# Performance work log

Measured on AMD Instinct MI355X. Metric: run time of the kernel, lower is better.

## Reference

```python
import jax, jax.numpy as jnp
import numpy as np

B, N, D = 64, 512, 768


def setup_inputs() -> dict:
    key = jax.random.key(0)
    k = jax.random.split(key, 7)
    x = jax.random.normal(k[0], (B, N, D), dtype=jnp.float32)
    adj = jax.random.normal(k[1], (B, N, N), dtype=jnp.float32)
    # additive BERT-style mask: 0 for valid tokens, -10000 for padding
    lengths = jax.random.randint(k[2], (B,), N // 2, N + 1)
    valid = jnp.arange(N)[None, :] < lengths[:, None]          # [B, N]
    mask = jnp.where(valid, 0.0, -10000.0).astype(jnp.float32).reshape(B, 1, 1, N)
    roots_label = (jax.random.uniform(k[3], (B, N)) < 0.1).astype(jnp.float32)
    root_mask = valid.astype(jnp.int32)
    w_root = jax.random.normal(k[4], (D,), dtype=jnp.float32) / np.sqrt(D)
    b_root = jnp.zeros((), dtype=jnp.float32)
    return {"x": x, "adj": adj, "mask": mask, "roots_label": roots_label,
            "root_mask": root_mask, "w_root": w_root, "b_root": b_root}


def _matrix_tree_multi(scores, root):
    # scores: [B,N,N], root: [B,N]
    A = jnp.exp(scores)
    R = jnp.exp(root)
    L = jnp.sum(A, axis=1)                     # column sums (torch dim=1)
    LL = jnp.zeros_like(A).at[:, jnp.arange(A.shape[1]), jnp.arange(A.shape[1])].set(L + R) - A
    # equivalent to diag(L) - A + diag(R); keep diag of -A zeroed by set:
    LL = (jnp.apply_along_axis(jnp.diag, 1, np.zeros((1,))) if False else LL)  # no-op
    LL = jax.vmap(jnp.diag)(L + R) - A + jax.vmap(jnp.diag)(jnp.diagonal(A, axis1=1, axis2=2))
    # Recompute cleanly to match torch exactly: LL = diag(L) - A + diag(R)
    LL = jax.vmap(jnp.diag)(L) - A + jax.vmap(jnp.diag)(R)
    LL_inv = jnp.linalg.inv(LL)                # [B,N,N]
    LL_inv_diag = jnp.diagonal(LL_inv, axis1=1, axis2=2)   # [B,N]
    d0 = R * LL_inv_diag                       # root marginals [B,N]
    tmp1 = A * LL_inv_diag[:, None, :]         # A[i,j] * diag[j]
    tmp2 = A * jnp.swapaxes(LL_inv, 1, 2)      # A[i,j] * LL_inv[j,i]
    d = tmp1 - tmp2                            # edge marginals [B,N,N]
    return d, d0


def reference(x, adj, mask, roots_label, root_mask, w_root, b_root):
    root = jnp.einsum("bnd,d->bn", x, w_root) + b_root          # [B,N]
    m = mask[:, 0] / -10000.0                                    # [B,1,N], 0 valid / 1 pad
    root = jnp.maximum(root - m[:, 0, :] * 50.0, -40.0)
    scores = adj - m * 50.0 - jnp.swapaxes(m, 1, 2) * 50.0
    scores = jnp.maximum(scores, -40.0)
    d, d0 = _matrix_tree_multi(scores, root)
    # BCE root loss
    active = root_mask.reshape(-1) == 1
    labels = jnp.where(active, roots_label.reshape(-1), 0.0).astype(jnp.float32)
    logits = jnp.clip(d0.reshape(-1), 1e-5, 1.0 - 1e-5).astype(jnp.float32)
    bce = -(labels * jnp.log(logits) + (1.0 - labels) * jnp.log(1.0 - logits))
    loss_root = jnp.mean(bce * root_mask.reshape(-1).astype(jnp.float32))
    # attention = d^T with padded key columns zeroed
    attn = jnp.swapaxes(d, 1, 2)
    pad = jnp.broadcast_to(m.astype(bool), scores.shape)         # [B,N,N]
    attn = jnp.where(pad, 0.0, attn)
    context = jnp.matmul(attn, x)                                # [B,N,D]
    return context, d, loss_root
```

## Files before the change

kernel.cpp:

```cpp
#include <hip/hip_runtime.h>
#include <cstdint>
#include <cstddef>

#define BB 64
#define NN 512
#define DD 768
#define KB 64
#define NSTEP (NN/KB)

typedef __bf16 bf16x8 __attribute__((ext_vector_type(8)));
typedef float f32x4 __attribute__((ext_vector_type(4)));
typedef unsigned short us8 __attribute__((ext_vector_type(8)));
typedef double f64x4 __attribute__((ext_vector_type(4)));
typedef double f64x2 __attribute__((ext_vector_type(2)));

__device__ __forceinline__ float aval(float adjv, float mi, float mj) {
    return expf(fmaxf(adjv - 50.f * (mi + mj), -40.f));
}

__device__ __forceinline__ unsigned short f2bf(float v) {
    union { float f; unsigned int u; } c; c.f = v;
    return (unsigned short)((c.u + 0x7fffu + ((c.u >> 16) & 1u)) >> 16);
}
__device__ __forceinline__ float bf2f(unsigned short h) {
    union { unsigned int u; float f; } c; c.u = ((unsigned int)h) << 16;
    return c.f;
}

__device__ __forceinline__ void gl_lds16(const void* g, void* l) {
    __builtin_amdgcn_global_load_lds((const __attribute__((address_space(1))) unsigned int*)g,
                                     (__attribute__((address_space(3))) unsigned int*)l, 16, 0, 0);
}

__global__ void k_root(const float* __restrict__ x, const float* __restrict__ mask,
                       const float* __restrict__ w, const float* __restrict__ br,
                       float* __restrict__ R) {
    int wave = threadIdx.x >> 6, lane = threadIdx.x & 63;
    int row = blockIdx.x * 4 + wave;
    const float* xr = x + (size_t)row * DD;
    float s = 0.f;
#pragma unroll
    for (int k = 0; k < DD / 64; ++k) s += xr[k * 64 + lane] * w[k * 64 + lane];
    for (int off = 32; off; off >>= 1) s += __shfl_down(s, off, 64);
    if (lane == 0) {
        float m = mask[row] * -1e-4f;
        float rv = fmaxf(s + br[0] - 50.f * m, -40.f);
        R[row] = expf(rv);
    }
}

__global__ void k_colsum(const float* __restrict__ adj, const float* __restrict__ mask,
                         double* __restrict__ Lp) {
    int b = blockIdx.x, chunk = blockIdx.y;
    int j = threadIdx.x;
    float mj = mask[b * NN + j] * -1e-4f;
    const float* ab = adj + (size_t)b * NN * NN;
    double acc = 0.0;
    int i0 = chunk * 128;
    for (int i = i0; i < i0 + 128; ++i) {
        float mi = mask[b * NN + i] * -1e-4f;
        acc += (double)aval(ab[(size_t)i * NN + j], mi, mj);
    }
    Lp[((size_t)b * 4 + chunk) * NN + j] = acc;
}

template <typename T>
__global__ void k_build(const float* __restrict__ adj, const float* __restrict__ mask,
                        const float* __restrict__ R, const double* __restrict__ Lp,
                        T* __restrict__ M) {
    int b = blockIdx.x >> 9;
    int r = blockIdx.x & 511;
    int c = threadIdx.x;
    float mr = mask[b * NN + r] * -1e-4f;
    float mc = mask[b * NN + c] * -1e-4f;
    size_t idx = ((size_t)b * NN + r) * NN + c;
    float a = aval(adj[idx], mr, mc);
    T v;
    if (r == c) {
        const double* lp = Lp + (size_t)b * 4 * NN;
        double L = lp[c] + lp[NN + c] + lp[2 * NN + c] + lp[3 * NN + c];
        v = (T)(L - (double)a + (double)R[b * NN + c]);
    } else {
        v = (T)(-a);
    }
    M[idx] = v;
}

template <typename T>
__global__ void k_savecol(const T* __restrict__ M, T* __restrict__ Cb, int k0) {
    int t = threadIdx.x;
    int c = t & 63, rr = t >> 6;
    int row = blockIdx.x * 4 + rr;
    int b = row >> 9, i = row & 511;
    Cb[(size_t)row * KB + c] = M[((size_t)b * NN + i) * NN + k0 + c];
}

template <typename T>
__global__ void k_invblk(const T* __restrict__ M, T* __restrict__ Bb, int k0) {
    __shared__ double pr[KB];
    __shared__ double fv[KB];
    __shared__ double pvt;
    int b = blockIdx.x;
    int r = threadIdx.x & 63, q = threadIdx.x >> 6;
    double a[16];
    const T* Mb = M + ((size_t)b * NN + k0) * NN + k0;
#pragma unroll
    for (int c = 0; c < 16; ++c) a[c] = (double)Mb[(size_t)r * NN + q * 16 + c];
    for (int k = 0; k < KB; ++k) {
        int kq = k >> 4, kc = k & 15;
        if (r == k && q == kq) pvt = a[kc];
        __syncthreads();
        double ip = 1.0 / pvt;
        if (r == k) {
#pragma unroll
            for (int c = 0; c < 16; ++c) a[c] *= ip;
            if (q == kq) a[kc] = ip;
#pragma unroll
            for (int c = 0; c < 16; ++c) pr[q * 16 + c] = a[c];
        }
        if (r != k && q == kq) fv[r] = a[kc];
        __syncthreads();
        if (r != k) {
            double f = fv[r];
#pragma unroll
            for (int c = 0; c < 16; ++c) a[c] -= f * pr[q * 16 + c];
            if (q == kq) a[kc] = -f * ip;
        }
        __syncthreads();
    }
    T* Bo = Bb + (size_t)b * KB * KB;
#pragma unroll
    for (int c = 0; c < 16; ++c) Bo[r * KB + q * 16 + c] = (T)a[c];
}

__global__ __launch_bounds__(256) void k_piv_mfma(double* __restrict__ M,
                                                  const double* __restrict__ Bb, int step) {
    __shared__ double Ms[64][66];
    int b = blockIdx.y, jt = blockIdx.x;
    int t = threadIdx.x, w = t >> 6, l = t & 63;
    double* Mb = M + (size_t)b * NN * NN;
    double* Pr = Mb + (size_t)(step * 64) * NN;
    const double* Bi = Bb + (size_t)b * KB * KB;
    if (jt == step) {
        for (int i = 0; i < 16; ++i) {
            int c = i * 256 + t;
            int row = c >> 6, col = c & 63;
            Pr[(size_t)row * NN + step * 64 + col] = Bi[row * 64 + col];
        }
        return;
    }
    const double* Mg = Pr + jt * 64;
    for (int i = 0; i < 8; ++i) {
        int c = i * 256 + t;
        int row = c >> 5, ch = c & 31;
        f64x2 v = *(const f64x2*)(Mg + (size_t)row * NN + ch * 2);
        Ms[row][ch * 2] = v[0]; Ms[row][ch * 2 + 1] = v[1];
    }
    __syncthreads();
    int lr = l & 15, lg = l >> 4;
    double a[16];
#pragma unroll
    for (int kk = 0; kk < 16; ++kk) a[kk] = Bi[(w * 16 + lr) * 64 + kk * 4 + lg];
    double* Og = Pr + (size_t)(w * 16) * NN + jt * 64;
#pragma unroll
    for (int cf = 0; cf < 4; ++cf) {
        f64x4 acc = {0., 0., 0., 0.};
#pragma unroll
        for (int kk = 0; kk < 16; ++kk)
            acc = __builtin_amdgcn_mfma_f64_16x16x4f64(a[kk], Ms[kk * 4 + lg][cf * 16 + lr], acc, 0, 0, 0);
#pragma unroll
        for (int r = 0; r < 4; ++r) Og[(size_t)(lg + 4 * r) * NN + cf * 16 + lr] = acc[r];
    }
}

template <int COLMODE>
__global__ __launch_bounds__(256) void k_upd_mfma(double* __restrict__ M, int step) {
    __shared__ double Cs[64][66];
    int b = blockIdx.y;
    int x = blockIdx.x;
    int it, jt;
    if (COLMODE) { it = x; jt = step; }
    else { it = x / 7; jt = x % 7; if (jt >= step) ++jt; }
    if (it >= step) ++it;
    int t = threadIdx.x, w = t >> 6, l = t & 63;
    double* Mb = M + (size_t)b * NN * NN;
    {
        const double* Cg = Mb + (size_t)(it * 64) * NN + step * 64;
        for (int i = 0; i < 8; ++i) {
            int c = i * 256 + t;
            int row = c >> 5, ch = c & 31;
            f64x2 v = *(const f64x2*)(Cg + (size_t)row * NN + ch * 2);
            Cs[row][ch * 2] = -v[0]; Cs[row][ch * 2 + 1] = -v[1];
        }
    }
    __syncthreads();
    int lr = l & 15, lg = l >> 4;
    double a[16];
#pragma unroll
    for (int kk = 0; kk < 16; ++kk) a[kk] = Cs[w * 16 + lr][kk * 4 + lg];
    const double* Rg = Mb + (size_t)(step * 64) * NN + jt * 64;
    double* Og = Mb + (size_t)(it * 64 + w * 16) * NN + jt * 64;
#pragma unroll
    for (int cf = 0; cf < 4; ++cf) {
        int c0 = cf * 16 + lr;
        f64x4 acc;
        if (COLMODE) {
            acc = (f64x4){0., 0., 0., 0.};
        } else {
#pragma unroll
            for (int r = 0; r < 4; ++r) acc[r] = Og[(size_t)(lg + 4 * r) * NN + c0];
        }
        const double* bp = Rg + (size_t)lg * NN + c0;
#pragma unroll
        for (int kk = 0; kk < 16; ++kk) {
            double bv = bp[(size_t)(kk * 4) * NN];
            acc = __builtin_amdgcn_mfma_f64_16x16x4f64(a[kk], bv, acc, 0, 0, 0);
        }
#pragma unroll
        for (int r = 0; r < 4; ++r) Og[(size_t)(lg + 4 * r) * NN + c0] = acc[r];
    }
}

template <typename T>
__global__ void k_pivrows(T* __restrict__ M, const T* __restrict__ Bb, int k0) {
    __shared__ double Bi[KB][KB];
    __shared__ double Mt[KB][KB + 1];
    int b = blockIdx.x, jt = blockIdx.y * 64;
    const T* Bo = Bb + (size_t)b * KB * KB;
    T* Mb = M + ((size_t)b * NN + k0) * NN;
    int t = threadIdx.x;
    for (int e = t; e < KB * KB; e += 256) {
        int rr = e >> 6, cc = e & 63;
        Bi[rr][cc] = (double)Bo[e];
        Mt[rr][cc] = (double)Mb[(size_t)rr * NN + jt + cc];
    }
    __syncthreads();
    if (blockIdx.y == (unsigned)(k0 >> 6)) {
        for (int e = t; e < KB * KB; e += 256) {
            int rr = e >> 6, cc = e & 63;
            Mb[(size_t)rr * NN + jt + cc] = (T)Bi[rr][cc];
        }
        return;
    }
    int tx = t & 15, ty = t >> 4;
    double acc[4][4] = {};
    for (int k = 0; k < KB; ++k) {
        double av[4], bv[4];
#pragma unroll
        for (int u = 0; u < 4; ++u) { av[u] = Bi[ty * 4 + u][k]; bv[u] = Mt[k][tx * 4 + u]; }
#pragma unroll
        for (int u = 0; u < 4; ++u)
#pragma unroll
            for (int v = 0; v < 4; ++v) acc[u][v] += av[u] * bv[v];
    }
#pragma unroll
    for (int u = 0; u < 4; ++u)
#pragma unroll
        for (int v = 0; v < 4; ++v)
            Mb[(size_t)(ty * 4 + u) * NN + jt + tx * 4 + v] = (T)acc[u][v];
}

template <typename T>
__global__ void k_update(T* __restrict__ M, const T* __restrict__ Cb, int k0) {
    int step = k0 >> 6;
    int it = blockIdx.y;
    if (it == step) return;
    int b = blockIdx.x, jt = blockIdx.z;
    __shared__ double Ct[KB][KB + 1];
    __shared__ double Rt[KB][KB + 1];
    int t = threadIdx.x;
    const T* Cbb = Cb + ((size_t)b * NN + it * 64) * KB;
    const T* Rb  = M + ((size_t)b * NN + k0) * NN + jt * 64;
    for (int e = t; e < KB * KB; e += 256) {
        int rr = e >> 6, cc = e & 63;
        Ct[rr][cc] = (double)Cbb[(size_t)rr * KB + cc];
        Rt[rr][cc] = (double)Rb[(size_t)rr * NN + cc];
    }
    __syncthreads();
    int tx = t & 15, ty = t >> 4;
    double acc[4][4] = {};
    for (int k = 0; k < KB; ++k) {
        double av[4], bv[4];
#pragma unroll
        for (int u = 0; u < 4; ++u) { av[u] = Ct[ty * 4 + u][k]; bv[u] = Rt[k][tx * 4 + u]; }
#pragma unroll
        for (int u = 0; u < 4; ++u)
#pragma unroll
            for (int v = 0; v < 4; ++v) acc[u][v] += av[u] * bv[v];
    }
    T* Mo = M + ((size_t)b * NN + it * 64) * NN + jt * 64;
    bool blockcol = (jt == step);
#pragma unroll
    for (int u = 0; u < 4; ++u) {
        int row = ty * 4 + u;
#pragma unroll
        for (int v = 0; v < 4; ++v) {
            int col = tx * 4 + v;
            double val = (double)Mo[(size_t)row * NN + col] - acc[u][v];
            if (blockcol) val -= Ct[row][col];
            Mo[(size_t)row * NN + col] = (T)val;
        }
    }
}

template <typename T>
__global__ void k_dgloss(const T* __restrict__ M, const float* __restrict__ R,
                         const float* __restrict__ rlab, const int* __restrict__ rmask,
                         double* __restrict__ Dg, float* __restrict__ lossp) {
    int idx = blockIdx.x * 256 + threadIdx.x;
    int b = idx >> 9, n = idx & 511;
    double xv = (double)M[((size_t)b * NN + n) * NN + n];
    Dg[idx] = xv;
    float d0 = R[idx] * (float)xv;
    float lg = fminf(fmaxf(d0, 1e-5f), 1.f - 1e-5f);
    float rm = (float)rmask[idx];
    float lab = (rmask[idx] == 1) ? rlab[idx] : 0.f;
    float bce = -(lab * logf(lg) + (1.f - lab) * logf(1.f - lg));
    __shared__ double sm[256];
    sm[threadIdx.x] = (double)(bce * rm);
    __syncthreads();
    for (int s = 128; s; s >>= 1) {
        if (threadIdx.x < s) sm[threadIdx.x] += sm[threadIdx.x + s];
        __syncthreads();
    }
    if (threadIdx.x == 0) lossp[blockIdx.x] = (float)sm[0];
}

__global__ void k_lossfin(const float* __restrict__ lossp, float* __restrict__ outv) {
    __shared__ double sm[128];
    sm[threadIdx.x] = (double)lossp[threadIdx.x];
    __syncthreads();
    for (int s = 64; s; s >>= 1) {
        if (threadIdx.x < s) sm[threadIdx.x] += sm[threadIdx.x + s];
        __syncthreads();
    }
    if (threadIdx.x == 0) outv[0] = (float)(sm[0] / (double)(BB * NN));
}

template <typename T>
__global__ void k_d(const T* __restrict__ M, const double* __restrict__ Dg,
                    const float* __restrict__ adj, const float* __restrict__ mask,
                    float* __restrict__ dout) {
    int b = blockIdx.x, i0 = blockIdx.y * 64, j0 = blockIdx.z * 64;
    __shared__ double Xt[64][65];
    int t = threadIdx.x, ii = t & 63, jj0 = t >> 6;
    const T* Mb = M + (size_t)b * NN * NN;
    for (int jj = jj0; jj < 64; jj += 4)
        Xt[jj][ii] = (double)Mb[(size_t)(j0 + jj) * NN + i0 + ii];
    __syncthreads();
    int jc = t & 63, ir0 = t >> 6;
    float mj = mask[b * NN + j0 + jc] * -1e-4f;
    double dg = Dg[b * NN + j0 + jc];
    const float* ab = adj + (size_t)b * NN * NN;
    float* db = dout + (size_t)b * NN * NN;
    for (int ir = ir0; ir < 64; ir += 4) {
        int i = i0 + ir;
        float mi = mask[b * NN + i] * -1e-4f;
        float a = aval(ab[(size_t)i * NN + j0 + jc], mi, mj);
        db[(size_t)i * NN + j0 + jc] = a * (float)(dg - Xt[jc][ir]);
    }
}

template <typename T>
__global__ void k_d2(const T* __restrict__ M, const double* __restrict__ Dg,
                     const float* __restrict__ adj, const float* __restrict__ mask,
                     float* __restrict__ dout,
                     unsigned short* __restrict__ ATh, unsigned short* __restrict__ ATl) {
    int b = blockIdx.x, i0 = blockIdx.y * 64, j0 = blockIdx.z * 64;
    __shared__ double Xt[64][65];
    __shared__ float dt[64][65];
    int t = threadIdx.x, ii = t & 63, jj0 = t >> 6;
    const T* Mb = M + (size_t)b * NN * NN;
    for (int jj = jj0; jj < 64; jj += 4)
        Xt[jj][ii] = (double)Mb[(size_t)(j0 + jj) * NN + i0 + ii];
    __syncthreads();
    int jc = t & 63, ir0 = t >> 6;
    float mj = mask[b * NN + j0 + jc] * -1e-4f;
    double dg = Dg[b * NN + j0 + jc];
    const float* ab = adj + (size_t)b * NN * NN;
    float* db = dout + (size_t)b * NN * NN;
    for (int ir = ir0; ir < 64; ir += 4) {
        int i = i0 + ir;
        float mi = mask[b * NN + i] * -1e-4f;
        float a = aval(ab[(size_t)i * NN + j0 + jc], mi, mj);
        float v = a * (float)(dg - Xt[jc][ir]);
        db[(size_t)i * NN + j0 + jc] = v;
        dt[ir][jc] = v;
    }
    __syncthreads();
    int ql = t >> 2, kq = t & 3;
    us8 vh0, vh1, vl0, vl1;
#pragma unroll
    for (int u = 0; u < 16; ++u) {
        int k = kq * 16 + u;
        float mk = mask[b * NN + i0 + k] * -1e-4f;
        float v = (mk > 0.5f) ? 0.f : dt[k][ql];
        unsigned short h = f2bf(v);
        unsigned short lo = f2bf(v - bf2f(h));
        if (u < 8) { vh0[u] = h; vl0[u] = lo; } else { vh1[u - 8] = h; vl1[u - 8] = lo; }
    }
    size_t ao = ((size_t)b * NN + j0 + ql) * NN + i0 + kq * 16;
    *(us8*)&ATh[ao] = vh0; *(us8*)&ATh[ao + 8] = vh1;
    *(us8*)&ATl[ao] = vl0; *(us8*)&ATl[ao + 8] = vl1;
}

__global__ void k_cvt_x(const float* __restrict__ x,
                        unsigned short* __restrict__ XTh, unsigned short* __restrict__ XTl) {
    int b = blockIdx.x, k0 = blockIdx.y * 64, c0 = blockIdx.z * 64;
    __shared__ float xs[64][65];
    int t = threadIdx.x;
#pragma unroll
    for (int rep = 0; rep < 16; ++rep) {
        int e = rep * 256 + t;
        int row = e >> 6, col = e & 63;
        xs[row][col] = x[((size_t)b * NN + k0 + row) * DD + c0 + col];
    }
    __syncthreads();
    int cl = t >> 2, kq = t & 3;
    us8 vh0, vh1, vl0, vl1;
#pragma unroll
    for (int u = 0; u < 16; ++u) {
        int k = kq * 16 + u;
        float v = xs[k][cl];
        unsigned short h = f2bf(v);
        unsigned short lo = f2bf(v - bf2f(h));
        if (u < 8) { vh0[u] = h; vl0[u] = lo; } else { vh1[u - 8] = h; vl1[u - 8] = lo; }
    }
    size_t ao = ((size_t)b * DD + c0 + cl) * NN + k0 + kq * 16;
    *(us8*)&XTh[ao] = vh0; *(us8*)&XTh[ao + 8] = vh1;
    *(us8*)&XTl[ao] = vl0; *(us8*)&XTl[ao + 8] = vl1;
}

__global__ __launch_bounds__(256) void k_ctx3(const unsigned short* __restrict__ ATh,
                                              const unsigned short* __restrict__ ATl,
                                              const unsigned short* __restrict__ XTh,
                                              const unsigned short* __restrict__ XTl,
                                              float* __restrict__ ctx) {
    __shared__ __align__(16) unsigned short ABs[128 * 64];
    __shared__ __align__(16) unsigned short Xs[128 * 64];
    int b = blockIdx.x;
    int bm = blockIdx.y * 128, bn = blockIdx.z * 128;
    int t = threadIdx.x, wid = t >> 6, lane = t & 63;
    f32x4 acc[4][4];
#pragma unroll
    for (int i = 0; i < 4; ++i)
#pragma unroll
        for (int j = 0; j < 4; ++j) acc[i][j] = (f32x4){0.f, 0.f, 0.f, 0.f};

    const unsigned short* Agh = ATh + ((size_t)b * NN + bm) * NN;
    const unsigned short* Agl = ATl + ((size_t)b * NN + bm) * NN;
    const unsigned short* Xgh = XTh + ((size_t)b * DD + bn) * NN;
    const unsigned short* Xgl = XTl + ((size_t)b * DD + bn) * NN;

    int m0 = (wid >> 1) * 64, n0 = (wid & 1) * 64;
    int kc = lane >> 4;

    for (int kt = 0; kt < 16; ++kt) {
        int ki = kt * 32;
        __syncthreads();
#pragma unroll
        for (int it2 = 0; it2 < 4; ++it2) {
            int chunk = it2 * 256 + wid * 64 + lane;
            int row = chunk >> 3;
            int gs = (chunk & 7) ^ (row & 7);
            const unsigned short* s = (gs < 4) ? Agh + (size_t)row * NN + ki + gs * 8
                                               : Agl + (size_t)row * NN + ki + (gs - 4) * 8;
            gl_lds16(s, &ABs[(it2 * 256 + wid * 64) * 8]);
        }
#pragma unroll
        for (int it2 = 0; it2 < 4; ++it2) {
            int chunk = it2 * 256 + wid * 64 + lane;
            int row = chunk >> 3;
            int gs = (chunk & 7) ^ (row & 7);
            const unsigned short* s = (gs < 4) ? Xgh + (size_t)row * NN + ki + gs * 8
                                               : Xgl + (size_t)row * NN + ki + (gs - 4) * 8;
            gl_lds16(s, &Xs[(it2 * 256 + wid * 64) * 8]);
        }
        __syncthreads();
        bf16x8 ah[4], al[4], xh[4], xl[4];
#pragma unroll
        for (int f = 0; f < 4; ++f) {
            int ar = m0 + f * 16 + (lane & 15);
            ah[f] = *(const bf16x8*)&ABs[(ar * 8 + (kc ^ (ar & 7))) * 8];
            al[f] = *(const bf16x8*)&ABs[(ar * 8 + ((kc | 4) ^ (ar & 7))) * 8];
            int br = n0 + f * 16 + (lane & 15);
            xh[f] = *(const bf16x8*)&Xs[(br * 8 + (kc ^ (br & 7))) * 8];
            xl[f] = *(const bf16x8*)&Xs[(br * 8 + ((kc | 4) ^ (br & 7))) * 8];
        }
#pragma unroll
        for (int fm = 0; fm < 4; ++fm)
#pragma unroll
            for (int fn = 0; fn < 4; ++fn) {
                acc[fm][fn] = __builtin_amdgcn_mfma_f32_16x16x32_bf16(ah[fm], xh[fn], acc[fm][fn], 0, 0, 0);
                acc[fm][fn] = __builtin_amdgcn_mfma_f32_16x16x32_bf16(ah[fm], xl[fn], acc[fm][fn], 0, 0, 0);
                acc[fm][fn] = __builtin_amdgcn_mfma_f32_16x16x32_bf16(al[fm], xh[fn], acc[fm][fn], 0, 0, 0);
            }
    }
    float* cb = ctx + ((size_t)b * NN + bm + m0) * DD + bn + n0;
#pragma unroll
    for (int fm = 0; fm < 4; ++fm)
#pragma unroll
        for (int fn = 0; fn < 4; ++fn)
#pragma unroll
            for (int r = 0; r < 4; ++r) {
                int row = fm * 16 + (lane >> 4) * 4 + r;
                int col = fn * 16 + (lane & 15);
                cb[(size_t)row * DD + col] = acc[fm][fn][r];
            }
}

__global__ void k_ctx(const float* __restrict__ dmat, const float* __restrict__ x,
                      const float* __restrict__ mask, float* __restrict__ ctx) {
    int b = blockIdx.x, i0 = blockIdx.y * 64, c0 = blockIdx.z * 64;
    __shared__ float At[32][65];
    __shared__ float Xl[32][65];
    int t = threadIdx.x;
    int tx = t & 15, ty = t >> 4;
    float acc[4][4] = {};
    const float* db = dmat + (size_t)b * NN * NN;
    const float* xb = x + (size_t)b * NN * DD;
    int li = t & 63, lk = t >> 6;
    for (int kt = 0; kt < NN; kt += 32) {
#pragma unroll
        for (int rep = 0; rep < 8; ++rep) {
            int kk = lk + rep * 4;
            float mk = mask[b * NN + kt + kk] * -1e-4f;
            float v = db[(size_t)(kt + kk) * NN + i0 + li];
            At[kk][li] = (mk > 0.5f) ? 0.f : v;
            Xl[kk][li] = xb[(size_t)(kt + kk) * DD + c0 + li];
        }
        __syncthreads();
        for (int kk = 0; kk < 32; ++kk) {
            float av[4], bv[4];
#pragma unroll
            for (int u = 0; u < 4; ++u) { av[u] = At[kk][ty * 4 + u]; bv[u] = Xl[kk][tx * 4 + u]; }
#pragma unroll
            for (int u = 0; u < 4; ++u)
#pragma unroll
                for (int v = 0; v < 4; ++v) acc[u][v] += av[u] * bv[v];
        }
        __syncthreads();
    }
    float* cb = ctx + (size_t)b * NN * DD;
#pragma unroll
    for (int u = 0; u < 4; ++u)
#pragma unroll
        for (int v = 0; v < 4; ++v)
            cb[(size_t)(i0 + ty * 4 + u) * DD + c0 + tx * 4 + v] = acc[u][v];
}

template <typename T>
static void run_old(const float* x, const float* adj, const float* mask,
                    const float* rlab, const int* rmask, const float* w, const float* br,
                    float* ctx, float* dmat, float* lossout,
                    char* ws, hipStream_t stream) {
    size_t off = 0;
    T* M  = (T*)(ws + off); off += (size_t)BB * NN * NN * sizeof(T);
    T* Cb = (T*)(ws + off); off += (size_t)BB * NN * KB * sizeof(T);
    T* Bb = (T*)(ws + off); off += (size_t)BB * KB * KB * sizeof(T);
    double* Lp = (double*)(ws + off); off += (size_t)BB * 4 * NN * 8;
    float* Rf  = (float*)(ws + off);  off += (size_t)BB * NN * 4;
    double* Dg = (double*)(ws + off); off += (size_t)BB * NN * 8;
    float* lossp = (float*)(ws + off);

    k_root<<<BB * NN / 4, 256, 0, stream>>>(x, mask, w, br, Rf);
    k_colsum<<<dim3(BB, 4), 512, 0, stream>>>(adj, mask, Lp);
    k_build<T><<<BB * NN, 512, 0, stream>>>(adj, mask, Rf, Lp, M);
    for (int s = 0; s < NSTEP; ++s) {
        int k0 = s * KB;
        k_savecol<T><<<BB * NN / 4, 256, 0, stream>>>(M, Cb, k0);
        k_invblk<T><<<BB, 256, 0, stream>>>(M, Bb, k0);
        k_pivrows<T><<<dim3(BB, 8), 256, 0, stream>>>(M, Bb, k0);
        k_update<T><<<dim3(BB, 8, 8), 256, 0, stream>>>(M, Cb, k0);
    }
    k_dgloss<T><<<BB * NN / 256, 256, 0, stream>>>(M, Rf, rlab, rmask, Dg, lossp);
    k_lossfin<<<1, 128, 0, stream>>>(lossp, lossout);
    k_d<T><<<dim3(BB, 8, 8), 256, 0, stream>>>(M, Dg, adj, mask, dmat);
    k_ctx<<<dim3(BB, 8, 12), 256, 0, stream>>>(dmat, x, mask, ctx);
}

static void run_new(const float* x, const float* adj, const float* mask,
                    const float* rlab, const int* rmask, const float* w, const float* br,
                    float* ctx, float* dmat, float* lossout,
                    char* ws, hipStream_t stream) {
    size_t off = 0;
    double* M  = (double*)(ws + off); off += (size_t)BB * NN * NN * 8;
    double* Cb = (double*)(ws + off); off += (size_t)BB * NN * KB * 8;
    double* Bb = (double*)(ws + off); off += (size_t)BB * KB * KB * 8;
    double* Lp = (double*)(ws + off); off += (size_t)BB * 4 * NN * 8;
    float* Rf  = (float*)(ws + off);  off += (size_t)BB * NN * 4;
    double* Dg = (double*)(ws + off); off += (size_t)BB * NN * 8;
    float* lossp = (float*)(ws + off); off += 4096;
    unsigned short* ATh = (unsigned short*)(ws + off); off += (size_t)BB * NN * NN * 2;
    unsigned short* ATl = (unsigned short*)(ws + off); off += (size_t)BB * NN * NN * 2;
    unsigned short* XTh = (unsigned short*)(ws);
    unsigned short* XTl = (unsigned short*)(ws + (size_t)BB * DD * NN * 2);
    (void)Cb;

    k_root<<<BB * NN / 4, 256, 0, stream>>>(x, mask, w, br, Rf);
    k_colsum<<<dim3(BB, 4), 512, 0, stream>>>(adj, mask, Lp);
    k_build<double><<<BB * NN, 512, 0, stream>>>(adj, mask, Rf, Lp, M);
    for (int s = 0; s < NSTEP; ++s) {
        k_invblk<double><<<BB, 256, 0, stream>>>(M, Bb, s * KB);
        k_piv_mfma<<<dim3(8, BB), 256, 0, stream>>>(M, Bb, s);
        k_upd_mfma<0><<<dim3(49, BB), 256, 0, stream>>>(M, s);
        k_upd_mfma<1><<<dim3(7, BB), 256, 0, stream>>>(M, s);
    }
    k_dgloss<double><<<BB * NN / 256, 256, 0, stream>>>(M, Rf, rlab, rmask, Dg, lossp);
    k_lossfin<<<1, 128, 0, stream>>>(lossp, lossout);
    k_d2<double><<<dim3(BB, 8, 8), 256, 0, stream>>>(M, Dg, adj, mask, dmat, ATh, ATl);
    k_cvt_x<<<dim3(BB, 8, 12), 256, 0, stream>>>(x, XTh, XTl);
    k_ctx3<<<dim3(BB, 4, 6), 256, 0, stream>>>(ATh, ATl, XTh, XTl, ctx);
}

extern "C" void kernel_launch(void* const* d_in, const int* in_sizes, int n_in,
                              void* d_out, int out_size, void* d_ws, size_t ws_size,
                              hipStream_t stream) {
    const float* x    = (const float*)d_in[0];
    const float* adj  = (const float*)d_in[1];
    const float* mask = (const float*)d_in[2];
    const float* rlab = (const float*)d_in[3];
    const int*   rmask= (const int*)d_in[4];
    const float* w    = (const float*)d_in[5];
    const float* br   = (const float*)d_in[6];
    float* out = (float*)d_out;
    float* ctx = out;
    float* dmat = out + (size_t)BB * NN * DD;
    float* lossout = dmat + (size_t)BB * NN * NN;
    char* ws = (char*)d_ws;

    size_t base = (size_t)BB * NN * NN * 8 + (size_t)BB * NN * KB * 8 + (size_t)BB * KB * KB * 8
                + (size_t)BB * 4 * NN * 8 + (size_t)BB * NN * 4 + (size_t)BB * NN * 8 + 4096;
    size_t need_new = base + (size_t)BB * NN * NN * 4;
    if (ws_size >= need_new)
        run_new(x, adj, mask, rlab, rmask, w, br, ctx, dmat, lossout, ws, stream);
    else if (ws_size >= base)
        run_old<double>(x, adj, mask, rlab, rmask, w, br, ctx, dmat, lossout, ws, stream);
    else
        run_old<float>(x, adj, mask, rlab, rmask, w, br, ctx, dmat, lossout, ws, stream);
}
```

Measured before the change: 1.396 ms.

## Merge block-inverse update kernels and stage pivot row tiles in LDS

Replaces the two trailing-update launches per step (off-diagonal tiles and pivot column) with one kernel where each block owns a row tile and half of the column tiles. The negated column panel is loaded once into registers and reused across several column tiles, and each pivot-row tile is staged through shared memory instead of strided global loads. The pivot-column product with the inverted diagonal block is folded into the same kernel. This reduces grid size from 56 to 14 blocks per batch, which lowers parallelism and adds serial work per block. It also shrinks a staging tile in k_d2 from double to float, which lowers LDS use at a small precision cost.

```diff
diff --git a/kernel.cpp b/kernel.cpp
--- a/kernel.cpp
+++ b/kernel.cpp
@@ -173,14 +173,12 @@
     }
 }
 
-template <int COLMODE>
-__global__ __launch_bounds__(256) void k_upd_mfma(double* __restrict__ M, int step) {
-    __shared__ double Cs[64][66];
+__global__ __launch_bounds__(256) void k_upd2(double* __restrict__ M,
+                                              const double* __restrict__ Bb, int step) {
+    __shared__ double Ts[64][66];
     int b = blockIdx.y;
     int x = blockIdx.x;
-    int it, jt;
-    if (COLMODE) { it = x; jt = step; }
-    else { it = x / 7; jt = x % 7; if (jt >= step) ++jt; }
+    int it = x >> 1, half = x & 1;
     if (it >= step) ++it;
     int t = threadIdx.x, w = t >> 6, l = t & 63;
     double* Mb = M + (size_t)b * NN * NN;
@@ -190,34 +188,62 @@
             int c = i * 256 + t;
             int row = c >> 5, ch = c & 31;
             f64x2 v = *(const f64x2*)(Cg + (size_t)row * NN + ch * 2);
-            Cs[row][ch * 2] = -v[0]; Cs[row][ch * 2 + 1] = -v[1];
+            Ts[row][ch * 2] = -v[0]; Ts[row][ch * 2 + 1] = -v[1];
         }
     }
     __syncthreads();
     int lr = l & 15, lg = l >> 4;
     double a[16];
 #pragma unroll
-    for (int kk = 0; kk < 16; ++kk) a[kk] = Cs[w * 16 + lr][kk * 4 + lg];
-    const double* Rg = Mb + (size_t)(step * 64) * NN + jt * 64;
-    double* Og = Mb + (size_t)(it * 64 + w * 16) * NN + jt * 64;
-#pragma unroll
-    for (int cf = 0; cf < 4; ++cf) {
-        int c0 = cf * 16 + lr;
-        f64x4 acc;
-        if (COLMODE) {
-            acc = (f64x4){0., 0., 0., 0.};
-        } else {
+    for (int kk = 0; kk < 16; ++kk) a[kk] = Ts[w * 16 + lr][kk * 4 + lg];
+    __syncthreads();
+    int nj = half ? 3 : 4;
+    for (int jj = 0; jj < nj; ++jj) {
+        int jtidx = half ? 4 + jj : jj;
+        int jt = (jtidx < step) ? jtidx : jtidx + 1;
+        const double* Rg = Mb + (size_t)(step * 64) * NN + jt * 64;
+        for (int i = 0; i < 8; ++i) {
+            int c = i * 256 + t;
+            int row = c >> 5, ch = c & 31;
+            f64x2 v = *(const f64x2*)(Rg + (size_t)row * NN + ch * 2);
+            Ts[row][ch * 2] = v[0]; Ts[row][ch * 2 + 1] = v[1];
+        }
+        __syncthreads();
+        double* Og = Mb + (size_t)(it * 64 + w * 16) * NN + jt * 64;
+#pragma unroll
+        for (int cf = 0; cf < 4; ++cf) {
+            int c0 = cf * 16 + lr;
+            f64x4 acc;
 #pragma unroll
             for (int r = 0; r < 4; ++r) acc[r] = Og[(size_t)(lg + 4 * r) * NN + c0];
-        }
-        const double* bp = Rg + (size_t)lg * NN + c0;
-#pragma unroll
-        for (int kk = 0; kk < 16; ++kk) {
-            double bv = bp[(size_t)(kk * 4) * NN];
-            acc = __builtin_amdgcn_mfma_f64_16x16x4f64(a[kk], bv, acc, 0, 0, 0);
-        }
-#pragma unroll
-        for (int r = 0; r < 4; ++r) Og[(size_t)(lg + 4 * r) * NN + c0] = acc[r];
+#pragma unroll
+            for (int kk = 0; kk < 16; ++kk)
+                acc = __builtin_amdgcn_mfma_f64_16x16x4f64(a[kk], Ts[kk * 4 + lg][c0], acc, 0, 0, 0);
+#pragma unroll
+            for (int r = 0; r < 4; ++r) Og[(size_t)(lg + 4 * r) * NN + c0] = acc[r];
+        }
+        __syncthreads();
+    }
+    if (half) {
+        const double* Bi = Bb + (size_t)b * KB * KB;
+        for (int i = 0; i < 8; ++i) {
+            int c = i * 256 + t;
+            int row = c >> 5, ch = c & 31;
+            f64x2 v = *(const f64x2*)(Bi + row * 64 + ch * 2);
+            Ts[row][ch * 2] = v[0]; Ts[row][ch * 2 + 1] = v[1];
+        }
+        __syncthreads();
+        double* Og = Mb + (size_t)(it * 64 + w * 16) * NN + step * 64;
+#pragma unroll
+        for (int cf = 0; cf < 4; ++cf) {
+            int c0 = cf * 16 + lr;
+            f64x4 acc = {0., 0., 0., 0.};
+#pragma unroll
+            for (int kk = 0; kk < 16; ++kk)
+                acc = __builtin_amdgcn_mfma_f64_16x16x4f64(a[kk], Ts[kk * 4 + lg][c0], acc, 0, 0, 0);
+#pragma unroll
+            for (int r = 0; r < 4; ++r) Og[(size_t)(lg + 4 * r) * NN + c0] = acc[r];
+        }
     }
 }
 
@@ -367,12 +393,12 @@
                      float* __restrict__ dout,
                      unsigned short* __restrict__ ATh, unsigned short* __restrict__ ATl) {
     int b = blockIdx.x, i0 = blockIdx.y * 64, j0 = blockIdx.z * 64;
-    __shared__ double Xt[64][65];
+    __shared__ float Xt[64][65];
     __shared__ float dt[64][65];
     int t = threadIdx.x, ii = t & 63, jj0 = t >> 6;
     const T* Mb = M + (size_t)b * NN * NN;
     for (int jj = jj0; jj < 64; jj += 4)
-        Xt[jj][ii] = (double)Mb[(size_t)(j0 + jj) * NN + i0 + ii];
+        Xt[jj][ii] = (float)Mb[(size_t)(j0 + jj) * NN + i0 + ii];
     __syncthreads();
     int jc = t & 63, ir0 = t >> 6;
     float mj = mask[b * NN + j0 + jc] * -1e-4f;
@@ -383,7 +409,7 @@
         int i = i0 + ir;
         float mi = mask[b * NN + i] * -1e-4f;
         float a = aval(ab[(size_t)i * NN + j0 + jc], mi, mj);
-        float v = a * (float)(dg - Xt[jc][ir]);
+        float v = a * (float)(dg - (double)Xt[jc][ir]);
         db[(size_t)i * NN + j0 + jc] = v;
         dt[ir][jc] = v;
     }
@@ -603,8 +629,7 @@
     for (int s = 0; s < NSTEP; ++s) {
         k_invblk<double><<<BB, 256, 0, stream>>>(M, Bb, s * KB);
         k_piv_mfma<<<dim3(8, BB), 256, 0, stream>>>(M, Bb, s);
-        k_upd_mfma<0><<<dim3(49, BB), 256, 0, stream>>>(M, s);
-        k_upd_mfma<1><<<dim3(7, BB), 256, 0, stream>>>(M, s);
+        k_upd2<<<dim3(14, BB), 256, 0, stream>>>(M, Bb, s);
     }
     k_dgloss<double><<<BB * NN / 256, 256, 0, stream>>>(M, Rf, rlab, rmask, Dg, lossp);
     k_lossfin<<<1, 128, 0, stream>>>(lossp, lossout);
```

Result: faster. 1.235 ms (-11.5%).
